# Optimization experiments

Measured on AMD Instinct MI355X. Metric: run time of the kernel, lower is better.

The kernel has to match this reference:

```python
import jax, jax.numpy as jnp
import numpy as np

N_NODES = 4096
N_GRAPHS = 128
D_IN = 128
HEADS = 4
KEY_SIZE = 32  # == num_channels
D_OUT = 32 * D_IN  # num_channels * irreps.dim


def setup_inputs() -> dict:
    key = jax.random.key(0)
    ks = jax.random.split(key, 5)
    nodes = jax.random.normal(ks[0], (N_NODES, D_IN), dtype=jnp.float32)
    # 128 graphs of 32 nodes each, packed: sum(n_node) == N_NODES
    n_node = jnp.full((N_GRAPHS,), N_NODES // N_GRAPHS, dtype=jnp.int32)
    s_in = 1.0 / np.sqrt(D_IN)
    s_h = 1.0 / np.sqrt(HEADS * KEY_SIZE)
    Wq = jax.random.normal(ks[1], (D_IN, HEADS, KEY_SIZE), dtype=jnp.float32) * s_in
    Wk = jax.random.normal(ks[2], (D_IN, HEADS, KEY_SIZE), dtype=jnp.float32) * s_in
    Wv = jax.random.normal(ks[3], (D_IN, HEADS, KEY_SIZE), dtype=jnp.float32) * s_in
    Wo = jax.random.normal(ks[4], (HEADS * KEY_SIZE, D_OUT), dtype=jnp.float32) * s_h
    bq = jnp.zeros((HEADS, KEY_SIZE), dtype=jnp.float32)
    bk = jnp.zeros((HEADS, KEY_SIZE), dtype=jnp.float32)
    bv = jnp.zeros((HEADS, KEY_SIZE), dtype=jnp.float32)
    bo = jnp.zeros((D_OUT,), dtype=jnp.float32)
    return {"nodes": nodes, "n_node": n_node, "Wq": Wq, "bq": bq,
            "Wk": Wk, "bk": bk, "Wv": Wv, "bv": bv, "Wo": Wo, "bo": bo}


def reference(nodes, n_node, Wq, bq, Wk, bk, Wv, bv, Wo, bo):
    N = nodes.shape[0]
    G = n_node.shape[0]
    # segment id per packed node (get_segment_ids)
    seg = jnp.repeat(jnp.arange(G), n_node, total_repeat_length=N)
    # per-head projections: [N, H, K]
    q = jnp.einsum('nd,dhk->nhk', nodes, Wq) + bq
    k = jnp.einsum('nd,dhk->nhk', nodes, Wk) + bk
    v = jnp.einsum('nd,dhk->nhk', nodes, Wv) + bv
    # dense logits masked to block-diagonal per-graph blocks: [H, N, N]
    logits = jnp.einsum('nhk,mhk->hnm', q, k) / jnp.sqrt(jnp.float32(KEY_SIZE))
    mask = seg[:, None] == seg[None, :]  # [N, N]
    logits = jnp.where(mask[None, :, :], logits, jnp.float32(-1e30))
    attn = jax.nn.softmax(logits, axis=-1)
    out = jnp.einsum('hnm,mhk->nhk', attn, v).reshape(N, HEADS * KEY_SIZE)
    return out @ Wo + bo  # [N, num_channels * d_in]
```

## Files before the change

kernel.cpp:

```cpp
#include <hip/hip_runtime.h>
#include <hip/hip_bf16.h>


typedef __attribute__((ext_vector_type(4))) float f32x4;
typedef __attribute__((ext_vector_type(8))) short s16x8;
typedef __attribute__((ext_vector_type(4))) short s16x4;
typedef __attribute__((ext_vector_type(8))) __bf16 bf16x8;

static __device__ __forceinline__ short f2bf(float f) {
  union { float f; unsigned u; } v; v.f = f;
  unsigned r = v.u + 0x7fffu + ((v.u >> 16) & 1u);
  return (short)(r >> 16);
}

static __device__ __forceinline__ f32x4 mfma16(s16x8 a, s16x8 b, f32x4 c) {
  return __builtin_amdgcn_mfma_f32_16x16x32_bf16(
      __builtin_bit_cast(bf16x8, a), __builtin_bit_cast(bf16x8, b), c, 0, 0, 0);
}

__global__ __launch_bounds__(256) void k0_prep(
    const float* __restrict__ Wq, const float* __restrict__ Wk,
    const float* __restrict__ Wv, const float* __restrict__ Wo,
    unsigned short* __restrict__ WqkvT, unsigned short* __restrict__ WoT)
{
  __shared__ alignas(16) short sT[64][136];
  const int b = blockIdx.x;
  const float* in; unsigned short* out; int C; int n0;
  if (b < 64)      { in = Wo; out = WoT;           C = 4096; n0 = b << 6; }
  else if (b < 66) { in = Wq; out = WqkvT;         C = 128;  n0 = (b - 64) << 6; }
  else if (b < 68) { in = Wk; out = WqkvT + 16384; C = 128;  n0 = (b - 66) << 6; }
  else             { in = Wv; out = WqkvT + 32768; C = 128;  n0 = (b - 68) << 6; }
  const int t  = threadIdx.x;
  const int rr = t >> 4;
  const int c4 = (t & 15) << 2;
  #pragma unroll
  for (int i = 0; i < 8; ++i) {
    int r = i * 16 + rr;
    float4 v = *(const float4*)(in + r * C + n0 + c4);
    sT[c4 + 0][r] = f2bf(v.x);
    sT[c4 + 1][r] = f2bf(v.y);
    sT[c4 + 2][r] = f2bf(v.z);
    sT[c4 + 3][r] = f2bf(v.w);
  }
  __syncthreads();
  const int c  = t >> 2;
  const int k0 = (t & 3) << 5;
  #pragma unroll
  for (int j = 0; j < 4; ++j)
    *(s16x8*)&out[(n0 + c) * 128 + k0 + j * 8] = *(const s16x8*)&sT[c][k0 + j * 8];
}

__global__ __launch_bounds__(64) void k1_qkv_attn(
    const float* __restrict__ nodes,
    const unsigned short* __restrict__ WqkvT,
    const float* __restrict__ bq, const float* __restrict__ bk,
    const float* __restrict__ bv,
    unsigned short* __restrict__ attout)
{
  const int g = blockIdx.x;
  const int h = blockIdx.y;
  const int lane = threadIdx.x;
  const int l15 = lane & 15;
  const int qd = lane >> 4;

  __shared__ alignas(16) short sN[32][136];
  __shared__ alignas(16) short sQ[32][40];
  __shared__ alignas(16) short sK[32][40];
  __shared__ alignas(16) short sVT[32][40];
  __shared__ alignas(16) short sP[32][40];

  const float* ng = nodes + g * 32 * 128;
  #pragma unroll
  for (int i = 0; i < 16; ++i) {
    int f4  = i * 64 + lane;
    int row = f4 >> 5;
    int c4  = (f4 & 31) << 2;
    float4 v = *(const float4*)(ng + row * 128 + c4);
    s16x4 p;
    p[0] = f2bf(v.x); p[1] = f2bf(v.y); p[2] = f2bf(v.z); p[3] = f2bf(v.w);
    *(s16x4*)&sN[row][c4] = p;
  }
  __syncthreads();

  s16x8 afrag[2][4];
  #pragma unroll
  for (int mt = 0; mt < 2; ++mt)
    #pragma unroll
    for (int kk = 0; kk < 4; ++kk)
      afrag[mt][kk] = *(const s16x8*)&sN[mt * 16 + l15][kk * 32 + qd * 8];

  const float* Bm[3] = {bq, bk, bv};

  #pragma unroll
  for (int m3 = 0; m3 < 3; ++m3) {
    const unsigned short* WT = WqkvT + m3 * 16384;
    s16x8 bfr[4][2];
    #pragma unroll
    for (int kk = 0; kk < 4; ++kk)
      #pragma unroll
      for (int nt = 0; nt < 2; ++nt)
        bfr[kk][nt] = *(const s16x8*)&WT[(h * 32 + nt * 16 + l15) * 128 + kk * 32 + qd * 8];
    f32x4 acc[2][2];
    f32x4 zero = {0.f, 0.f, 0.f, 0.f};
    acc[0][0] = zero; acc[0][1] = zero; acc[1][0] = zero; acc[1][1] = zero;
    #pragma unroll
    for (int kk = 0; kk < 4; ++kk)
      #pragma unroll
      for (int mt = 0; mt < 2; ++mt)
        #pragma unroll
        for (int nt = 0; nt < 2; ++nt)
          acc[mt][nt] = mfma16(afrag[mt][kk], bfr[kk][nt], acc[mt][nt]);
    float b0 = Bm[m3][h * 32 + l15];
    float b1 = Bm[m3][h * 32 + 16 + l15];
    #pragma unroll
    for (int mt = 0; mt < 2; ++mt)
      #pragma unroll
      for (int nt = 0; nt < 2; ++nt) {
        float bb = nt ? b1 : b0;
        #pragma unroll
        for (int r = 0; r < 4; ++r) {
          int m = mt * 16 + qd * 4 + r;
          int c = nt * 16 + l15;
          float val = acc[mt][nt][r] + bb;
          if (m3 == 0)      sQ[m][c]  = f2bf(val * 0.17677669529663687f);
          else if (m3 == 1) sK[m][c]  = f2bf(val);
          else              sVT[c][m] = f2bf(val);
        }
      }
  }
  __syncthreads();

  s16x8 qf[2], kf[2];
  #pragma unroll
  for (int mt = 0; mt < 2; ++mt) qf[mt] = *(const s16x8*)&sQ[mt * 16 + l15][qd * 8];
  #pragma unroll
  for (int nt = 0; nt < 2; ++nt) kf[nt] = *(const s16x8*)&sK[nt * 16 + l15][qd * 8];
  f32x4 sacc[2][2];
  {
    f32x4 zero = {0.f, 0.f, 0.f, 0.f};
    #pragma unroll
    for (int mt = 0; mt < 2; ++mt)
      #pragma unroll
      for (int nt = 0; nt < 2; ++nt)
        sacc[mt][nt] = mfma16(qf[mt], kf[nt], zero);
  }

  #pragma unroll
  for (int mt = 0; mt < 2; ++mt)
    #pragma unroll
    for (int r = 0; r < 4; ++r) {
      float a0 = sacc[mt][0][r], a1 = sacc[mt][1][r];
      float mx = fmaxf(a0, a1);
      mx = fmaxf(mx, __shfl_xor(mx, 1, 64));
      mx = fmaxf(mx, __shfl_xor(mx, 2, 64));
      mx = fmaxf(mx, __shfl_xor(mx, 4, 64));
      mx = fmaxf(mx, __shfl_xor(mx, 8, 64));
      float e0 = __expf(a0 - mx), e1 = __expf(a1 - mx);
      float s = e0 + e1;
      s += __shfl_xor(s, 1, 64);
      s += __shfl_xor(s, 2, 64);
      s += __shfl_xor(s, 4, 64);
      s += __shfl_xor(s, 8, 64);
      float inv = 1.0f / s;
      int m = mt * 16 + qd * 4 + r;
      sP[m][l15]      = f2bf(e0 * inv);
      sP[m][16 + l15] = f2bf(e1 * inv);
    }
  __syncthreads();

  s16x8 pf[2], vf[2];
  #pragma unroll
  for (int mt = 0; mt < 2; ++mt) pf[mt] = *(const s16x8*)&sP[mt * 16 + l15][qd * 8];
  #pragma unroll
  for (int nt = 0; nt < 2; ++nt) vf[nt] = *(const s16x8*)&sVT[nt * 16 + l15][qd * 8];
  f32x4 oacc[2][2];
  {
    f32x4 zero = {0.f, 0.f, 0.f, 0.f};
    #pragma unroll
    for (int mt = 0; mt < 2; ++mt)
      #pragma unroll
      for (int nt = 0; nt < 2; ++nt)
        oacc[mt][nt] = mfma16(pf[mt], vf[nt], zero);
  }
  unsigned short* ao = attout + (g * 32) * 128 + h * 32;
  #pragma unroll
  for (int mt = 0; mt < 2; ++mt)
    #pragma unroll
    for (int nt = 0; nt < 2; ++nt)
      #pragma unroll
      for (int r = 0; r < 4; ++r) {
        int m = mt * 16 + qd * 4 + r;
        int c = nt * 16 + l15;
        ao[m * 128 + c] = (unsigned short)f2bf(oacc[mt][nt][r]);
      }
}

__global__ __launch_bounds__(256) void k3_gemm(
    const unsigned short* __restrict__ A,
    const unsigned short* __restrict__ BT,
    const float* __restrict__ bo,
    float* __restrict__ C)
{
  __shared__ alignas(16) short sA[128][136];
  __shared__ alignas(16) short sB[128][136];
  const int t  = threadIdx.x;
  const int m0 = blockIdx.y << 7;
  const int n0 = blockIdx.x << 7;

  #pragma unroll
  for (int i = 0; i < 8; ++i) {
    int id  = i * 256 + t;
    int row = id >> 4;
    int ch  = (id & 15) << 3;
    *(s16x8*)&sA[row][ch] = *(const s16x8*)(A  + (m0 + row) * 128 + ch);
    *(s16x8*)&sB[row][ch] = *(const s16x8*)(BT + (n0 + row) * 128 + ch);
  }
  __syncthreads();

  const int w    = t >> 6;
  const int lane = t & 63;
  const int l15  = lane & 15;
  const int qd   = lane >> 4;
  const int wm   = (w >> 1) << 6;
  const int wn   = (w & 1) << 6;

  f32x4 acc[4][4];
  {
    f32x4 zero = {0.f, 0.f, 0.f, 0.f};
    #pragma unroll
    for (int j = 0; j < 4; ++j)
      #pragma unroll
      for (int i = 0; i < 4; ++i) acc[j][i] = zero;
  }

  #pragma unroll
  for (int kk = 0; kk < 4; ++kk) {
    s16x8 af[4], bf[4];
    #pragma unroll
    for (int i = 0; i < 4; ++i)
      af[i] = *(const s16x8*)&sA[wm + i * 16 + l15][kk * 32 + qd * 8];
    #pragma unroll
    for (int j = 0; j < 4; ++j)
      bf[j] = *(const s16x8*)&sB[wn + j * 16 + l15][kk * 32 + qd * 8];
    #pragma unroll
    for (int j = 0; j < 4; ++j)
      #pragma unroll
      for (int i = 0; i < 4; ++i)
        acc[j][i] = mfma16(bf[j], af[i], acc[j][i]);
  }

  f32x4 bv4[4];
  #pragma unroll
  for (int j = 0; j < 4; ++j)
    bv4[j] = *(const f32x4*)&bo[n0 + wn + j * 16 + qd * 4];

  #pragma unroll
  for (int i = 0; i < 4; ++i) {
    float* crow = C + (m0 + wm + i * 16 + l15) * 4096 + n0 + wn + qd * 4;
    #pragma unroll
    for (int j = 0; j < 4; ++j) {
      f32x4 v = acc[j][i] + bv4[j];
      *(f32x4*)(crow + j * 16) = v;
    }
  }
}

extern "C" void kernel_launch(void* const* d_in, const int* in_sizes, int n_in,
                              void* d_out, int out_size, void* d_ws, size_t ws_size,
                              hipStream_t stream) {
  const float* nodes = (const float*)d_in[0];
  const float* Wq = (const float*)d_in[2];
  const float* bq = (const float*)d_in[3];
  const float* Wk = (const float*)d_in[4];
  const float* bk = (const float*)d_in[5];
  const float* Wv = (const float*)d_in[6];
  const float* bv = (const float*)d_in[7];
  const float* Wo = (const float*)d_in[8];
  const float* bo = (const float*)d_in[9];
  float* out = (float*)d_out;

  unsigned short* attout = (unsigned short*)d_ws;
  unsigned short* WoT    = attout + 4096 * 128;
  unsigned short* WqkvT  = WoT + 4096 * 128;

  k0_prep<<<70, 256, 0, stream>>>(Wq, Wk, Wv, Wo, WqkvT, WoT);
  k1_qkv_attn<<<dim3(128, 4), 64, 0, stream>>>(nodes, WqkvT, bq, bk, bv, attout);
  k3_gemm<<<dim3(32, 32), 256, 0, stream>>>(attout, WoT, bo, out);
}
```

Before: 111.3 us.

## Pre-convert nodes to bf16 in prep kernel and split attention across two waves

The fp32-to-bf16 conversion of nodes moves into the prep kernel through 64 extra blocks, so it runs once instead of once per head. The attention kernel then loads A fragments for the QKV projection straight from global memory and drops the shared staging buffer and its barrier. Each attention block now runs two waves, each owning 16 query rows, which halves per-wave MFMA and softmax work. The barrier between softmax and the PV product is removed because each wave reads only its own sP rows. The cost is an extra bf16 workspace buffer and a longer prep kernel, while the large output GEMM still likely dominates total time.

```diff
diff --git a/kernel.cpp b/kernel.cpp
--- a/kernel.cpp
+++ b/kernel.cpp
@@ -19,18 +19,36 @@
 }
 
 __global__ __launch_bounds__(256) void k0_prep(
+    const float* __restrict__ nodes,
     const float* __restrict__ Wq, const float* __restrict__ Wk,
     const float* __restrict__ Wv, const float* __restrict__ Wo,
-    unsigned short* __restrict__ WqkvT, unsigned short* __restrict__ WoT)
+    unsigned short* __restrict__ WqkvT, unsigned short* __restrict__ WoT,
+    unsigned short* __restrict__ nodesBF)
 {
+  const int b = blockIdx.x;
+  const int t = threadIdx.x;
+
+  if (b >= 70) {
+    const int r0 = (b - 70) << 6;
+    const float* src = nodes + r0 * 128;
+    unsigned short* dst = nodesBF + r0 * 128;
+    #pragma unroll
+    for (int i = 0; i < 8; ++i) {
+      int idx = (i * 256 + t) << 2;
+      float4 v = *(const float4*)(src + idx);
+      s16x4 p;
+      p[0] = f2bf(v.x); p[1] = f2bf(v.y); p[2] = f2bf(v.z); p[3] = f2bf(v.w);
+      *(s16x4*)(dst + idx) = p;
+    }
+    return;
+  }
+
   __shared__ alignas(16) short sT[64][136];
-  const int b = blockIdx.x;
   const float* in; unsigned short* out; int C; int n0;
   if (b < 64)      { in = Wo; out = WoT;           C = 4096; n0 = b << 6; }
   else if (b < 66) { in = Wq; out = WqkvT;         C = 128;  n0 = (b - 64) << 6; }
   else if (b < 68) { in = Wk; out = WqkvT + 16384; C = 128;  n0 = (b - 66) << 6; }
   else             { in = Wv; out = WqkvT + 32768; C = 128;  n0 = (b - 68) << 6; }
-  const int t  = threadIdx.x;
   const int rr = t >> 4;
   const int c4 = (t & 15) << 2;
   #pragma unroll
@@ -50,8 +68,8 @@
     *(s16x8*)&out[(n0 + c) * 128 + k0 + j * 8] = *(const s16x8*)&sT[c][k0 + j * 8];
 }
 
-__global__ __launch_bounds__(64) void k1_qkv_attn(
-    const float* __restrict__ nodes,
+__global__ __launch_bounds__(128) void k1_qkv_attn(
+    const unsigned short* __restrict__ nodesBF,
     const unsigned short* __restrict__ WqkvT,
     const float* __restrict__ bq, const float* __restrict__ bk,
     const float* __restrict__ bv,
@@ -59,140 +77,110 @@
 {
   const int g = blockIdx.x;
   const int h = blockIdx.y;
-  const int lane = threadIdx.x;
-  const int l15 = lane & 15;
-  const int qd = lane >> 4;
-
-  __shared__ alignas(16) short sN[32][136];
+  const int t = threadIdx.x;
+  const int wv   = t >> 6;
+  const int lane = t & 63;
+  const int l15  = lane & 15;
+  const int qd   = lane >> 4;
+  const int mrow = wv << 4;
+
   __shared__ alignas(16) short sQ[32][40];
   __shared__ alignas(16) short sK[32][40];
   __shared__ alignas(16) short sVT[32][40];
   __shared__ alignas(16) short sP[32][40];
 
-  const float* ng = nodes + g * 32 * 128;
-  #pragma unroll
-  for (int i = 0; i < 16; ++i) {
-    int f4  = i * 64 + lane;
-    int row = f4 >> 5;
-    int c4  = (f4 & 31) << 2;
-    float4 v = *(const float4*)(ng + row * 128 + c4);
-    s16x4 p;
-    p[0] = f2bf(v.x); p[1] = f2bf(v.y); p[2] = f2bf(v.z); p[3] = f2bf(v.w);
-    *(s16x4*)&sN[row][c4] = p;
-  }
-  __syncthreads();
-
-  s16x8 afrag[2][4];
-  #pragma unroll
-  for (int mt = 0; mt < 2; ++mt)
+  s16x8 afrag[4];
+  const unsigned short* nb = nodesBF + (g * 32 + mrow + l15) * 128 + qd * 8;
+  #pragma unroll
+  for (int kk = 0; kk < 4; ++kk) afrag[kk] = *(const s16x8*)(nb + kk * 32);
+
+  s16x8 bfr[3][4][2];
+  #pragma unroll
+  for (int m3 = 0; m3 < 3; ++m3) {
+    const unsigned short* WT = WqkvT + m3 * 16384 + (h * 32 + l15) * 128 + qd * 8;
     #pragma unroll
     for (int kk = 0; kk < 4; ++kk)
-      afrag[mt][kk] = *(const s16x8*)&sN[mt * 16 + l15][kk * 32 + qd * 8];
-
+      #pragma unroll
+      for (int nt = 0; nt < 2; ++nt)
+        bfr[m3][kk][nt] = *(const s16x8*)(WT + nt * 16 * 128 + kk * 32);
+  }
   const float* Bm[3] = {bq, bk, bv};
 
   #pragma unroll
   for (int m3 = 0; m3 < 3; ++m3) {
-    const unsigned short* WT = WqkvT + m3 * 16384;
-    s16x8 bfr[4][2];
+    f32x4 acc[2];
+    f32x4 zero = {0.f, 0.f, 0.f, 0.f};
+    acc[0] = zero; acc[1] = zero;
     #pragma unroll
     for (int kk = 0; kk < 4; ++kk)
       #pragma unroll
       for (int nt = 0; nt < 2; ++nt)
-        bfr[kk][nt] = *(const s16x8*)&WT[(h * 32 + nt * 16 + l15) * 128 + kk * 32 + qd * 8];
-    f32x4 acc[2][2];
-    f32x4 zero = {0.f, 0.f, 0.f, 0.f};
-    acc[0][0] = zero; acc[0][1] = zero; acc[1][0] = zero; acc[1][1] = zero;
-    #pragma unroll
-    for (int kk = 0; kk < 4; ++kk)
-      #pragma unroll
-      for (int mt = 0; mt < 2; ++mt)
-        #pragma unroll
-        for (int nt = 0; nt < 2; ++nt)
-          acc[mt][nt] = mfma16(afrag[mt][kk], bfr[kk][nt], acc[mt][nt]);
+        acc[nt] = mfma16(afrag[kk], bfr[m3][kk][nt], acc[nt]);
     float b0 = Bm[m3][h * 32 + l15];
     float b1 = Bm[m3][h * 32 + 16 + l15];
     #pragma unroll
-    for (int mt = 0; mt < 2; ++mt)
-      #pragma unroll
-      for (int nt = 0; nt < 2; ++nt) {
-        float bb = nt ? b1 : b0;
-        #pragma unroll
-        for (int r = 0; r < 4; ++r) {
-          int m = mt * 16 + qd * 4 + r;
-          int c = nt * 16 + l15;
-          float val = acc[mt][nt][r] + bb;
-          if (m3 == 0)      sQ[m][c]  = f2bf(val * 0.17677669529663687f);
-          else if (m3 == 1) sK[m][c]  = f2bf(val);
-          else              sVT[c][m] = f2bf(val);
-        }
+    for (int nt = 0; nt < 2; ++nt) {
+      float bb = nt ? b1 : b0;
+      #pragma unroll
+      for (int r = 0; r < 4; ++r) {
+        int m = mrow + qd * 4 + r;
+        int c = nt * 16 + l15;
+        float val = acc[nt][r] + bb;
+        if (m3 == 0)      sQ[m][c]  = f2bf(val * 0.17677669529663687f);
+        else if (m3 == 1) sK[m][c]  = f2bf(val);
+        else              sVT[c][m] = f2bf(val);
       }
+    }
   }
   __syncthreads();
 
-  s16x8 qf[2], kf[2];
-  #pragma unroll
-  for (int mt = 0; mt < 2; ++mt) qf[mt] = *(const s16x8*)&sQ[mt * 16 + l15][qd * 8];
+  s16x8 qf = *(const s16x8*)&sQ[mrow + l15][qd * 8];
+  s16x8 kf[2];
   #pragma unroll
   for (int nt = 0; nt < 2; ++nt) kf[nt] = *(const s16x8*)&sK[nt * 16 + l15][qd * 8];
-  f32x4 sacc[2][2];
+  f32x4 sacc[2];
   {
     f32x4 zero = {0.f, 0.f, 0.f, 0.f};
-    #pragma unroll
-    for (int mt = 0; mt < 2; ++mt)
-      #pragma unroll
-      for (int nt = 0; nt < 2; ++nt)
-        sacc[mt][nt] = mfma16(qf[mt], kf[nt], zero);
-  }
-
-  #pragma unroll
-  for (int mt = 0; mt < 2; ++mt)
-    #pragma unroll
-    for (int r = 0; r < 4; ++r) {
-      float a0 = sacc[mt][0][r], a1 = sacc[mt][1][r];
-      float mx = fmaxf(a0, a1);
-      mx = fmaxf(mx, __shfl_xor(mx, 1, 64));
-      mx = fmaxf(mx, __shfl_xor(mx, 2, 64));
-      mx = fmaxf(mx, __shfl_xor(mx, 4, 64));
-      mx = fmaxf(mx, __shfl_xor(mx, 8, 64));
-      float e0 = __expf(a0 - mx), e1 = __expf(a1 - mx);
-      float s = e0 + e1;
-      s += __shfl_xor(s, 1, 64);
-      s += __shfl_xor(s, 2, 64);
-      s += __shfl_xor(s, 4, 64);
-      s += __shfl_xor(s, 8, 64);
-      float inv = 1.0f / s;
-      int m = mt * 16 + qd * 4 + r;
-      sP[m][l15]      = f2bf(e0 * inv);
-      sP[m][16 + l15] = f2bf(e1 * inv);
-    }
-  __syncthreads();
-
-  s16x8 pf[2], vf[2];
-  #pragma unroll
-  for (int mt = 0; mt < 2; ++mt) pf[mt] = *(const s16x8*)&sP[mt * 16 + l15][qd * 8];
+    sacc[0] = mfma16(qf, kf[0], zero);
+    sacc[1] = mfma16(qf, kf[1], zero);
+  }
+
+  #pragma unroll
+  for (int r = 0; r < 4; ++r) {
+    float a0 = sacc[0][r], a1 = sacc[1][r];
+    float mx = fmaxf(a0, a1);
+    mx = fmaxf(mx, __shfl_xor(mx, 1, 64));
+    mx = fmaxf(mx, __shfl_xor(mx, 2, 64));
+    mx = fmaxf(mx, __shfl_xor(mx, 4, 64));
+    mx = fmaxf(mx, __shfl_xor(mx, 8, 64));
+    float e0 = __expf(a0 - mx), e1 = __expf(a1 - mx);
+    float s = e0 + e1;
+    s += __shfl_xor(s, 1, 64);
+    s += __shfl_xor(s, 2, 64);
+    s += __shfl_xor(s, 4, 64);
+    s += __shfl_xor(s, 8, 64);
+    float inv = 1.0f / s;
+    int m = mrow + qd * 4 + r;
+    sP[m][l15]      = f2bf(e0 * inv);
+    sP[m][16 + l15] = f2bf(e1 * inv);
+  }
+
+  s16x8 pf = *(const s16x8*)&sP[mrow + l15][qd * 8];
+  s16x8 vf[2];
   #pragma unroll
   for (int nt = 0; nt < 2; ++nt) vf[nt] = *(const s16x8*)&sVT[nt * 16 + l15][qd * 8];
-  f32x4 oacc[2][2];
+  f32x4 oacc[2];
   {
     f32x4 zero = {0.f, 0.f, 0.f, 0.f};
-    #pragma unroll
-    for (int mt = 0; mt < 2; ++mt)
-      #pragma unroll
-      for (int nt = 0; nt < 2; ++nt)
-        oacc[mt][nt] = mfma16(pf[mt], vf[nt], zero);
-  }
-  unsigned short* ao = attout + (g * 32) * 128 + h * 32;
-  #pragma unroll
-  for (int mt = 0; mt < 2; ++mt)
-    #pragma unroll
-    for (int nt = 0; nt < 2; ++nt)
-      #pragma unroll
-      for (int r = 0; r < 4; ++r) {
-        int m = mt * 16 + qd * 4 + r;
-        int c = nt * 16 + l15;
-        ao[m * 128 + c] = (unsigned short)f2bf(oacc[mt][nt][r]);
-      }
+    oacc[0] = mfma16(pf, vf[0], zero);
+    oacc[1] = mfma16(pf, vf[1], zero);
+  }
+  unsigned short* ao = attout + (g * 32 + mrow) * 128 + h * 32;
+  #pragma unroll
+  for (int nt = 0; nt < 2; ++nt)
+    #pragma unroll
+    for (int r = 0; r < 4; ++r)
+      ao[(qd * 4 + r) * 128 + nt * 16 + l15] = (unsigned short)f2bf(oacc[nt][r]);
 }
 
 __global__ __launch_bounds__(256) void k3_gemm(
@@ -279,11 +267,12 @@
   const float* bo = (const float*)d_in[9];
   float* out = (float*)d_out;
 
-  unsigned short* attout = (unsigned short*)d_ws;
-  unsigned short* WoT    = attout + 4096 * 128;
-  unsigned short* WqkvT  = WoT + 4096 * 128;
-
-  k0_prep<<<70, 256, 0, stream>>>(Wq, Wk, Wv, Wo, WqkvT, WoT);
-  k1_qkv_attn<<<dim3(128, 4), 64, 0, stream>>>(nodes, WqkvT, bq, bk, bv, attout);
+  unsigned short* attout  = (unsigned short*)d_ws;
+  unsigned short* WoT     = attout + 4096 * 128;
+  unsigned short* WqkvT   = WoT + 4096 * 128;
+  unsigned short* nodesBF = WqkvT + 3 * 128 * 128;
+
+  k0_prep<<<134, 256, 0, stream>>>(nodes, Wq, Wk, Wv, Wo, WqkvT, WoT, nodesBF);
+  k1_qkv_attn<<<dim3(128, 4), 128, 0, stream>>>(nodesBF, WqkvT, bq, bk, bv, attout);
   k3_gemm<<<dim3(32, 32), 256, 0, stream>>>(attout, WoT, bo, out);
 }
```

New measurement: 112.0 us. Within noise of the previous version (+0.6%).
